# Performance work log

Hardware: AMD Instinct MI355X
Metric: run time of the kernel (lower is better)

## Reference

```python
import jax, jax.numpy as jnp
import numpy as np

CAPACITY = 2  # module init arg


def setup_inputs() -> dict:
    B, S, D, E, I = 4, 4096, 1024, 8, 4096
    key = jax.random.key(0)
    k0, k1, k2, k3, k4 = jax.random.split(key, 5)
    x = jax.random.normal(k0, (B, S, D), dtype=jnp.float32)
    # nn.init.normal_(gate_weight, std=0.006)
    gate_w = jax.random.normal(k1, (E, D), dtype=jnp.float32) * 0.006
    w_gate = jax.random.normal(k2, (E, I, D), dtype=jnp.float32) * (1.0 / np.sqrt(D))
    w_up = jax.random.normal(k3, (E, I, D), dtype=jnp.float32) * (1.0 / np.sqrt(D))
    w_down = jax.random.normal(k4, (E, D, I), dtype=jnp.float32) * (1.0 / np.sqrt(I))
    return {"x": x, "gate_w": gate_w, "w_gate": w_gate, "w_up": w_up, "w_down": w_down}


def reference(x, gate_w, w_gate, w_up, w_down):
    # Expert-choice MoE. The torch code materializes a one-hot dispatch tensor
    # (B,E,C,S) and contracts it with x / x_e; mathematically that is exactly an
    # indexed gather (dispatch) and scatter-add (combine), which we do directly.
    B, S, D = x.shape
    E = gate_w.shape[0]
    k = (S // E) * CAPACITY  # capacity per expert

    logits = jnp.einsum('bsd,ed->bse', x, gate_w)
    affinity = jax.nn.softmax(logits, axis=-1)              # softmax over experts
    affinity = jnp.transpose(affinity, (0, 2, 1))           # (B,E,S)
    gating, idx = jax.lax.top_k(affinity, k)                # each expert picks k tokens; (B,E,k)

    bidx = jnp.arange(B)[:, None, None]                     # (B,1,1) broadcast vs (B,E,k)
    x_in = x[bidx, idx]                                     # gather: (B,E,k,D)

    # per-expert gated SiLU MLP: down(silu(gate(x)) * up(x))
    h = jax.nn.silu(jnp.einsum('bekd,eid->beki', x_in, w_gate)) \
        * jnp.einsum('bekd,eid->beki', x_in, w_up)          # (B,E,k,I)
    x_e = jnp.einsum('beki,edi->bekd', h, w_down)           # (B,E,k,D)

    # combine: scatter-add gated expert outputs back to token positions
    out = jnp.zeros_like(x).at[bidx, idx].add(gating[..., None] * x_e)
    return out
```

## Files before the change

kernel.cpp:

```cpp
#include <hip/hip_runtime.h>
#include <hip/hip_bf16.h>


#define B_ 4
#define S_ 4096
#define D_ 1024
#define E_ 8
#define I_ 4096
#define KCAP 1024
#define NGROUPS 32

typedef __bf16 bf16x8 __attribute__((ext_vector_type(8)));
typedef float floatx4 __attribute__((ext_vector_type(4)));

#define GLD16(gptr, lptr)                                          \
  __builtin_amdgcn_global_load_lds(                                \
      (const __attribute__((address_space(1))) void*)(gptr),       \
      (__attribute__((address_space(3))) void*)(lptr), 16, 0, 0)

#define WAITV(N) asm volatile("s_waitcnt vmcnt(" #N ")" ::: "memory")
#define RAW_BAR() __builtin_amdgcn_s_barrier()
#define CFENCE() asm volatile("" ::: "memory")

__device__ __forceinline__ float bf2f(unsigned short h) {
  union { unsigned int u; float f; } v; v.u = ((unsigned int)h) << 16; return v.f;
}
__device__ __forceinline__ unsigned short f2bf(float f) {
  union { float f; unsigned int u; } v; v.f = f;
  unsigned int r = (v.u + 0x7fffu + ((v.u >> 16) & 1u)) >> 16;
  return (unsigned short)r;
}

__global__ __launch_bounds__(256) void probe_dtype_k(const unsigned short* __restrict__ xr,
                                                     int* __restrict__ flag) {
  __shared__ unsigned int cnt;
  if (threadIdx.x == 0) cnt = 0;
  __syncthreads();
  unsigned int local = 0;
  for (int j = 0; j < 16; ++j) {
    int k = threadIdx.x * 16 + j;
    unsigned short u = xr[2 * k];
    unsigned int expf = (u >> 7) & 0xFF;
    if (expf >= 0x90 && expf != 0xFF) local++;
    if (expf == 0xFF) local++;
  }
  atomicAdd(&cnt, local);
  __syncthreads();
  if (threadIdx.x == 0) *flag = (cnt > 256u) ? 1 : 0;
}

__global__ __launch_bounds__(256) void conv_in_k(const void* __restrict__ src,
                                                 unsigned short* __restrict__ dst,
                                                 const int* __restrict__ flag) {
  const int isf32 = *flag;
  size_t i = ((size_t)blockIdx.x * 256 + threadIdx.x) * 8;
  if (isf32) {
    const float* s = (const float*)src;
    float4 a = *(const float4*)(s + i);
    float4 b = *(const float4*)(s + i + 4);
    ushort4 o0, o1;
    o0.x = f2bf(a.x); o0.y = f2bf(a.y); o0.z = f2bf(a.z); o0.w = f2bf(a.w);
    o1.x = f2bf(b.x); o1.y = f2bf(b.y); o1.z = f2bf(b.z); o1.w = f2bf(b.w);
    *(ushort4*)(dst + i) = o0;
    *(ushort4*)(dst + i + 4) = o1;
  } else {
    const uint4* s = (const uint4*)src;
    *(uint4*)(dst + i) = s[i / 8];
  }
}

__global__ __launch_bounds__(256) void gate_softmax_k(
    const void* __restrict__ xr, const void* __restrict__ gwr,
    const int* __restrict__ flag, double* __restrict__ aff) {
  const int isf32 = *flag;
  const int wave = threadIdx.x >> 6, lane = threadIdx.x & 63;
  const int token = blockIdx.x * 4 + wave;
  double acc[E_];
#pragma unroll
  for (int e2 = 0; e2 < E_; ++e2) acc[e2] = 0.0;
  for (int j = 0; j < 16; ++j) {
    int k = lane + 64 * j;
    double xv, wv[E_];
    if (isf32) {
      xv = (double)((const float*)xr)[(size_t)token * D_ + k];
#pragma unroll
      for (int e2 = 0; e2 < E_; ++e2) wv[e2] = (double)((const float*)gwr)[e2 * D_ + k];
    } else {
      xv = (double)bf2f(((const unsigned short*)xr)[(size_t)token * D_ + k]);
#pragma unroll
      for (int e2 = 0; e2 < E_; ++e2) wv[e2] = (double)bf2f(((const unsigned short*)gwr)[e2 * D_ + k]);
    }
#pragma unroll
    for (int e2 = 0; e2 < E_; ++e2) acc[e2] += xv * wv[e2];
  }
#pragma unroll
  for (int e2 = 0; e2 < E_; ++e2) {
#pragma unroll
    for (int off = 1; off < 64; off <<= 1) acc[e2] += __shfl_xor(acc[e2], off);
  }
  if (lane < E_) {
    double mx = acc[0];
#pragma unroll
    for (int e2 = 1; e2 < E_; ++e2) mx = acc[e2] > mx ? acc[e2] : mx;
    double ssum = 0.0;
#pragma unroll
    for (int e2 = 0; e2 < E_; ++e2) ssum += exp(acc[e2] - mx);
    double p = exp(acc[lane] - mx) / ssum;
    int b = token >> 12, s = token & (S_ - 1);
    aff[((size_t)b * E_ + lane) * S_ + s] = p;
  }
}

__global__ __launch_bounds__(256) void topk_sel_k(
    const double* __restrict__ aff, int* __restrict__ sel_idx, float* __restrict__ sel_gate) {
  __shared__ unsigned long long keys[4096];
  __shared__ unsigned int hist[256];
  __shared__ unsigned int bcast[3];
  const int g = blockIdx.x, t = threadIdx.x;
  const int e = g >> 2, b = g & 3;
  const double* ap = aff + ((size_t)b * E_ + e) * S_;
  for (int j = 0; j < 16; ++j) {
    int i = t + 256 * j;
    keys[i] = __double_as_longlong(ap[i]);
  }
  __syncthreads();
  unsigned long long prefix = 0ull;
  int remaining = KCAP;
  for (int p = 7; p >= 0; --p) {
    hist[t] = 0;
    __syncthreads();
    unsigned long long mask_hi = (p == 7) ? 0ull : (~0ull << ((p + 1) * 8));
    for (int j = 0; j < 16; ++j) {
      unsigned long long key = keys[t + 256 * j];
      if ((key & mask_hi) == prefix)
        atomicAdd(&hist[(unsigned)(key >> (p * 8)) & 255u], 1u);
    }
    __syncthreads();
    if (t == 0) {
      unsigned cum = 0; int bsel = 0;
      for (int v = 255; v >= 0; --v) {
        unsigned cc = hist[v];
        if (cum + cc >= (unsigned)remaining) { bsel = v; break; }
        cum += cc;
      }
      bcast[0] = (unsigned)bsel; bcast[1] = cum;
    }
    __syncthreads();
    prefix |= ((unsigned long long)bcast[0]) << (p * 8);
    remaining -= (int)bcast[1];
    __syncthreads();
  }
  if (t == 0) bcast[2] = 0;
  __syncthreads();
  const unsigned long long T = prefix;
  for (int j = 0; j < 16; ++j) {
    int i = t + 256 * j;
    unsigned long long key = keys[i];
    if (key > T) {
      unsigned pos = atomicAdd(&bcast[2], 1u);
      sel_idx[g * KCAP + pos] = i;
      sel_gate[g * KCAP + pos] = (float)__longlong_as_double(key);
    }
  }
  __syncthreads();
  for (int j = 0; j < 16; ++j) {
    int i = t + 256 * j;
    unsigned long long key = keys[i];
    if (key == T) {
      unsigned pos = atomicAdd(&bcast[2], 1u);
      if (pos < KCAP) {
        sel_idx[g * KCAP + pos] = i;
        sel_gate[g * KCAP + pos] = (float)__longlong_as_double(key);
      }
    }
  }
}

__global__ __launch_bounds__(512, 2) void moe_gemm1(
    const unsigned short* __restrict__ x, const unsigned short* __restrict__ w_gate,
    const unsigned short* __restrict__ w_up, const int* __restrict__ sel_idx,
    unsigned short* __restrict__ hbuf, int chunk_start) {
  __shared__ __align__(16) unsigned short lds[4 * 16384];
  const int gc = blockIdx.z;
  const int g = chunk_start + gc;
  const int e = g >> 2, b = g & 3;
  const int lid = blockIdx.x;
  const int swz = (lid & 7) * 16 + (lid >> 3);
  const int m0 = (swz & 3) * 256, n0 = (swz >> 2) * 128;
  const int t = threadIdx.x;
  const int wave = t >> 6, lane = t & 63;
  const int wm = wave >> 2, wn = wave & 3;
  const int row16 = lane & 15, quad = lane >> 4;

  const int atok = sel_idx[g * KCAP + m0 + (t & 255)] & (S_ - 1);
  const unsigned short* gA = x + ((size_t)b * S_ + atok) * D_ + (t >> 8) * 8;
  const unsigned short* gG = w_gate + ((size_t)e * I_ + n0 + (t & 127)) * D_ + (t >> 7) * 8;
  const unsigned short* gU = w_up + ((size_t)e * I_ + n0 + (t & 127)) * D_ + (t >> 7) * 8;

  floatx4 accg[8][2], accu[8][2];
#pragma unroll
  for (int m = 0; m < 8; ++m)
#pragma unroll
    for (int n = 0; n < 2; ++n) {
      accg[m][n] = (floatx4){0.f, 0.f, 0.f, 0.f};
      accu[m][n] = (floatx4){0.f, 0.f, 0.f, 0.f};
    }

#define STG1(KT, SL) do {                                   \
    unsigned short* sb_ = lds + (SL) * 16384;               \
    const int k0_ = (KT) * 32;                              \
    GLD16(gA + k0_,      sb_ + wave * 512);                 \
    GLD16(gA + k0_ + 16, sb_ + 4096 + wave * 512);          \
    GLD16(gG + k0_,      sb_ + 8192 + wave * 512);          \
    GLD16(gU + k0_,      sb_ + 12288 + wave * 512);         \
  } while (0)

#define COMP1(SL) do {                                                              \
    const unsigned short* sb_ = lds + (SL) * 16384;                                 \
    bf16x8 af[8], gf[2], uf[2];                                                     \
    _Pragma("unroll")                                                               \
    for (int m = 0; m < 8; ++m)                                                     \
      af[m] = *(const bf16x8*)(sb_ + (quad * 256 + wm * 128 + m * 16 + row16) * 8); \
    _Pragma("unroll")                                                               \
    for (int n = 0; n < 2; ++n) {                                                   \
      gf[n] = *(const bf16x8*)(sb_ + 8192 + (quad * 128 + wn * 32 + n * 16 + row16) * 8);  \
      uf[n] = *(const bf16x8*)(sb_ + 12288 + (quad * 128 + wn * 32 + n * 16 + row16) * 8); \
    }                                                                               \
    __builtin_amdgcn_s_setprio(1);                                                  \
    _Pragma("unroll")                                                               \
    for (int m = 0; m < 8; ++m)                                                     \
      _Pragma("unroll")                                                             \
      for (int n = 0; n < 2; ++n) {                                                 \
        accg[m][n] = __builtin_amdgcn_mfma_f32_16x16x32_bf16(af[m], gf[n], accg[m][n], 0, 0, 0); \
        accu[m][n] = __builtin_amdgcn_mfma_f32_16x16x32_bf16(af[m], uf[n], accu[m][n], 0, 0, 0); \
      }                                                                             \
    __builtin_amdgcn_s_setprio(0);                                                  \
  } while (0)

  STG1(0, 0); CFENCE(); STG1(1, 1); CFENCE(); STG1(2, 2);
#pragma unroll 4
  for (int kt = 0; kt < 28; ++kt) {
    WAITV(8); RAW_BAR();
    STG1(kt + 3, (kt + 3) & 3);
    COMP1(kt & 3);
  }
  { WAITV(8); RAW_BAR(); STG1(31, 3); COMP1(0); }
  { WAITV(8); RAW_BAR(); COMP1(1); }
  { WAITV(4); RAW_BAR(); COMP1(2); }
  { WAITV(0); RAW_BAR(); COMP1(3); }
#undef STG1
#undef COMP1

  unsigned short* hb = hbuf + (size_t)gc * ((size_t)KCAP * I_);
#pragma unroll
  for (int m = 0; m < 8; ++m)
#pragma unroll
    for (int n = 0; n < 2; ++n)
#pragma unroll
      for (int r4 = 0; r4 < 4; ++r4) {
        int mm = m0 + wm * 128 + m * 16 + quad * 4 + r4;
        int nn = n0 + wn * 32 + n * 16 + row16;
        float gv = accg[m][n][r4], uv = accu[m][n][r4];
        float hv = gv / (1.f + __expf(-gv)) * uv;
        hb[(size_t)mm * I_ + nn] = f2bf(hv);
      }
}

__global__ __launch_bounds__(512, 2) void moe_gemm2(
    const unsigned short* __restrict__ hbuf, const unsigned short* __restrict__ w_down,
    const int* __restrict__ sel_idx, const float* __restrict__ sel_gate,
    float* __restrict__ acc_out, int chunk_start) {
  __shared__ __align__(16) unsigned short lds[4 * 16384];
  __shared__ int stok[256];
  __shared__ float sgt[256];
  const int gc = blockIdx.z;
  const int g = chunk_start + gc;
  const int e = g >> 2, b = g & 3;
  const int m0 = (blockIdx.x & 3) * 256, n0 = (blockIdx.x >> 2) * 256;
  const int t = threadIdx.x;
  const int wave = t >> 6, lane = t & 63;
  const int wm = wave >> 2, wn = wave & 3;
  const int row16 = lane & 15, quad = lane >> 4;

  if (t < 256) {
    stok[t] = sel_idx[g * KCAP + m0 + t] & (S_ - 1);
    sgt[t] = sel_gate[g * KCAP + m0 + t];
  }

  const unsigned short* gA = hbuf + (size_t)gc * ((size_t)KCAP * I_) +
                             (size_t)(m0 + (t & 255)) * I_ + (t >> 8) * 8;
  const unsigned short* gB = w_down + ((size_t)e * D_ + n0 + (t & 255)) * I_ + (t >> 8) * 8;

  floatx4 accf[8][4];
#pragma unroll
  for (int m = 0; m < 8; ++m)
#pragma unroll
    for (int n = 0; n < 4; ++n) accf[m][n] = (floatx4){0.f, 0.f, 0.f, 0.f};

#define STG2(KT, SL) do {                                   \
    unsigned short* sb_ = lds + (SL) * 16384;               \
    const int k0_ = (KT) * 32;                              \
    GLD16(gA + k0_,      sb_ + wave * 512);                 \
    GLD16(gA + k0_ + 16, sb_ + 4096 + wave * 512);          \
    GLD16(gB + k0_,      sb_ + 8192 + wave * 512);          \
    GLD16(gB + k0_ + 16, sb_ + 12288 + wave * 512);         \
  } while (0)

#define COMP2(SL) do {                                                              \
    const unsigned short* sb_ = lds + (SL) * 16384;                                 \
    bf16x8 af[8], bf[4];                                                            \
    _Pragma("unroll")                                                               \
    for (int m = 0; m < 8; ++m)                                                     \
      af[m] = *(const bf16x8*)(sb_ + (quad * 256 + wm * 128 + m * 16 + row16) * 8); \
    _Pragma("unroll")                                                               \
    for (int n = 0; n < 4; ++n)                                                     \
      bf[n] = *(const bf16x8*)(sb_ + 8192 + (quad * 256 + wn * 64 + n * 16 + row16) * 8); \
    __builtin_amdgcn_s_setprio(1);                                                  \
    _Pragma("unroll")                                                               \
    for (int m = 0; m < 8; ++m)                                                     \
      _Pragma("unroll")                                                             \
      for (int n = 0; n < 4; ++n)                                                   \
        accf[m][n] = __builtin_amdgcn_mfma_f32_16x16x32_bf16(af[m], bf[n], accf[m][n], 0, 0, 0); \
    __builtin_amdgcn_s_setprio(0);                                                  \
  } while (0)

  STG2(0, 0); CFENCE(); STG2(1, 1); CFENCE(); STG2(2, 2);
#pragma unroll 4
  for (int kt = 0; kt < 124; ++kt) {
    WAITV(8); RAW_BAR();
    STG2(kt + 3, (kt + 3) & 3);
    COMP2(kt & 3);
  }
  { WAITV(8); RAW_BAR(); STG2(127, 3); COMP2(0); }
  { WAITV(8); RAW_BAR(); COMP2(1); }
  { WAITV(4); RAW_BAR(); COMP2(2); }
  { WAITV(0); RAW_BAR(); COMP2(3); }
#undef STG2
#undef COMP2

#pragma unroll
  for (int m = 0; m < 8; ++m)
#pragma unroll
    for (int r4 = 0; r4 < 4; ++r4) {
      int mloc = wm * 128 + m * 16 + quad * 4 + r4;
      int tok = stok[mloc];
      float gt = sgt[mloc];
      float* basep = acc_out + ((size_t)b * S_ + tok) * D_ + n0 + wn * 64 + row16;
#pragma unroll
      for (int n = 0; n < 4; ++n) unsafeAtomicAdd(basep + n * 16, accf[m][n][r4] * gt);
    }
}

__global__ __launch_bounds__(256) void conv_out_k(const float* __restrict__ acc,
                                                  void* __restrict__ out,
                                                  const int* __restrict__ flag) {
  const int isf32 = *flag;
  size_t i = ((size_t)blockIdx.x * 256 + threadIdx.x) * 4;
  float4 v = *(const float4*)(acc + i);
  if (isf32) {
    *(float4*)((float*)out + i) = v;
  } else {
    ushort4 o;
    o.x = f2bf(v.x); o.y = f2bf(v.y); o.z = f2bf(v.z); o.w = f2bf(v.w);
    *(ushort4*)((unsigned short*)out + i) = o;
  }
}

extern "C" void kernel_launch(void* const* d_in, const int* in_sizes, int n_in,
                              void* d_out, int out_size, void* d_ws, size_t ws_size,
                              hipStream_t stream) {
  const void* x_raw = d_in[0];
  const void* gate_w_raw = d_in[1];
  const void* w_gate_raw = d_in[2];
  const void* w_up_raw = d_in[3];
  const void* w_down_raw = d_in[4];

  char* ws = (char*)d_ws;
  size_t off = 0;
  auto alloc = [&](size_t bytes) { char* p = ws + off; off += (bytes + 255) & ~(size_t)255; return p; };
  float* acc = (float*)alloc((size_t)B_ * S_ * D_ * 4);
  double* aff = (double*)alloc((size_t)B_ * E_ * S_ * 8);
  int* sel_idx = (int*)alloc((size_t)NGROUPS * KCAP * 4);
  float* sel_gate = (float*)alloc((size_t)NGROUPS * KCAP * 4);
  int* flag = (int*)alloc(256);
  unsigned short* xb = (unsigned short*)alloc((size_t)B_ * S_ * D_ * 2);
  unsigned short* wgb = (unsigned short*)alloc((size_t)E_ * I_ * D_ * 2);
  unsigned short* wub = (unsigned short*)alloc((size_t)E_ * I_ * D_ * 2);
  unsigned short* wdb = (unsigned short*)alloc((size_t)E_ * D_ * I_ * 2);
  const size_t fixedBytes = off;
  const size_t hPerGroup = (size_t)KCAP * I_ * 2;
  int gch = 32;
  while (gch > 1 && fixedBytes + (size_t)gch * hPerGroup > ws_size) gch >>= 1;
  unsigned short* hbuf = (unsigned short*)(ws + fixedBytes);

  hipMemsetAsync(acc, 0, (size_t)B_ * S_ * D_ * 4, stream);
  hipMemsetAsync(sel_idx, 0, (size_t)NGROUPS * KCAP * 8, stream);

  probe_dtype_k<<<dim3(1), dim3(256), 0, stream>>>((const unsigned short*)x_raw, flag);
  conv_in_k<<<dim3((int)((size_t)B_ * S_ * D_ / 2048)), dim3(256), 0, stream>>>(x_raw, xb, flag);
  conv_in_k<<<dim3((int)((size_t)E_ * I_ * D_ / 2048)), dim3(256), 0, stream>>>(w_gate_raw, wgb, flag);
  conv_in_k<<<dim3((int)((size_t)E_ * I_ * D_ / 2048)), dim3(256), 0, stream>>>(w_up_raw, wub, flag);
  conv_in_k<<<dim3((int)((size_t)E_ * D_ * I_ / 2048)), dim3(256), 0, stream>>>(w_down_raw, wdb, flag);

  gate_softmax_k<<<dim3(B_ * S_ / 4), dim3(256), 0, stream>>>(x_raw, gate_w_raw, flag, aff);
  topk_sel_k<<<dim3(NGROUPS), dim3(256), 0, stream>>>(aff, sel_idx, sel_gate);
  for (int c0 = 0; c0 < NGROUPS; c0 += gch) {
    int gcur = (NGROUPS - c0) < gch ? (NGROUPS - c0) : gch;
    moe_gemm1<<<dim3(128, 1, gcur), dim3(512), 0, stream>>>(
        xb, wgb, wub, sel_idx, hbuf, c0);
    moe_gemm2<<<dim3(16, 1, gcur), dim3(512), 0, stream>>>(
        hbuf, wdb, sel_idx, sel_gate, acc, c0);
  }
  conv_out_k<<<dim3((int)((size_t)B_ * S_ * D_ / 4 / 256)), dim3(256), 0, stream>>>(acc, d_out, flag);
}
```

Baseline: 1.951 ms.

## Split GEMM k-steps into two interleaved phases with staged loads and barriers

Both expert GEMM kernels now split each k-step into two half-tile MFMA phases. The global-to-LDS loads for a future stage are spread across the phases, and barriers plus explicit lgkmcnt waits and sched_barriers control the instruction order, in a ping-pong style schedule. Launch bounds drop from 2 to 1 block per CU, which frees registers but leaves fewer resident waves to hide latency. The tail iterations reload clamped k-slice 31/127 into spare slots, which adds redundant loads. The extra barriers per k-step add sync cost.

```diff
diff --git a/kernel.cpp b/kernel.cpp
--- a/kernel.cpp
+++ b/kernel.cpp
@@ -19,8 +19,11 @@
       (__attribute__((address_space(3))) void*)(lptr), 16, 0, 0)
 
 #define WAITV(N) asm volatile("s_waitcnt vmcnt(" #N ")" ::: "memory")
+#define LGKM0() do { asm volatile("s_waitcnt lgkmcnt(0)" ::: "memory"); \
+                     __builtin_amdgcn_sched_barrier(0); } while (0)
 #define RAW_BAR() __builtin_amdgcn_s_barrier()
 #define CFENCE() asm volatile("" ::: "memory")
+#define MFMA_BF16(A, Bb, C) __builtin_amdgcn_mfma_f32_16x16x32_bf16((A), (Bb), (C), 0, 0, 0)
 
 __device__ __forceinline__ float bf2f(unsigned short h) {
   union { unsigned int u; float f; } v; v.u = ((unsigned int)h) << 16; return v.f;
@@ -176,7 +179,7 @@
   }
 }
 
-__global__ __launch_bounds__(512, 2) void moe_gemm1(
+__global__ __launch_bounds__(512, 1) void moe_gemm1(
     const unsigned short* __restrict__ x, const unsigned short* __restrict__ w_gate,
     const unsigned short* __restrict__ w_up, const int* __restrict__ sel_idx,
     unsigned short* __restrict__ hbuf, int chunk_start) {
@@ -192,10 +195,10 @@
   const int wm = wave >> 2, wn = wave & 3;
   const int row16 = lane & 15, quad = lane >> 4;
 
-  const int atok = sel_idx[g * KCAP + m0 + (t & 255)] & (S_ - 1);
-  const unsigned short* gA = x + ((size_t)b * S_ + atok) * D_ + (t >> 8) * 8;
-  const unsigned short* gG = w_gate + ((size_t)e * I_ + n0 + (t & 127)) * D_ + (t >> 7) * 8;
-  const unsigned short* gU = w_up + ((size_t)e * I_ + n0 + (t & 127)) * D_ + (t >> 7) * 8;
+  const int tokA = sel_idx[g * KCAP + m0 + (t & 255)] & (S_ - 1);
+  const unsigned short* pA = x + ((size_t)b * S_ + tokA) * D_ + (t >> 8) * 8;
+  const unsigned short* pG = w_gate + ((size_t)e * I_ + n0 + (t & 127)) * D_ + (t >> 7) * 8;
+  const unsigned short* pU = w_up + ((size_t)e * I_ + n0 + (t & 127)) * D_ + (t >> 7) * 8;
 
   floatx4 accg[8][2], accu[8][2];
 #pragma unroll
@@ -205,51 +208,77 @@
       accg[m][n] = (floatx4){0.f, 0.f, 0.f, 0.f};
       accu[m][n] = (floatx4){0.f, 0.f, 0.f, 0.f};
     }
-
-#define STG1(KT, SL) do {                                   \
-    unsigned short* sb_ = lds + (SL) * 16384;               \
-    const int k0_ = (KT) * 32;                              \
-    GLD16(gA + k0_,      sb_ + wave * 512);                 \
-    GLD16(gA + k0_ + 16, sb_ + 4096 + wave * 512);          \
-    GLD16(gG + k0_,      sb_ + 8192 + wave * 512);          \
-    GLD16(gU + k0_,      sb_ + 12288 + wave * 512);         \
-  } while (0)
-
-#define COMP1(SL) do {                                                              \
-    const unsigned short* sb_ = lds + (SL) * 16384;                                 \
-    bf16x8 af[8], gf[2], uf[2];                                                     \
-    _Pragma("unroll")                                                               \
-    for (int m = 0; m < 8; ++m)                                                     \
-      af[m] = *(const bf16x8*)(sb_ + (quad * 256 + wm * 128 + m * 16 + row16) * 8); \
-    _Pragma("unroll")                                                               \
-    for (int n = 0; n < 2; ++n) {                                                   \
-      gf[n] = *(const bf16x8*)(sb_ + 8192 + (quad * 128 + wn * 32 + n * 16 + row16) * 8);  \
-      uf[n] = *(const bf16x8*)(sb_ + 12288 + (quad * 128 + wn * 32 + n * 16 + row16) * 8); \
-    }                                                                               \
-    __builtin_amdgcn_s_setprio(1);                                                  \
-    _Pragma("unroll")                                                               \
-    for (int m = 0; m < 8; ++m)                                                     \
-      _Pragma("unroll")                                                             \
-      for (int n = 0; n < 2; ++n) {                                                 \
-        accg[m][n] = __builtin_amdgcn_mfma_f32_16x16x32_bf16(af[m], gf[n], accg[m][n], 0, 0, 0); \
-        accu[m][n] = __builtin_amdgcn_mfma_f32_16x16x32_bf16(af[m], uf[n], accu[m][n], 0, 0, 0); \
-      }                                                                             \
-    __builtin_amdgcn_s_setprio(0);                                                  \
-  } while (0)
+  bf16x8 af[4], gf[2], uf[2];
+
+#define STG1(KT, SL) do { unsigned short* sb_ = lds + (SL) * 16384;  \
+    const int k0_ = (KT) * 32;                                       \
+    GLD16(pA + k0_,      sb_ + wave * 512);                          \
+    GLD16(pA + k0_ + 16, sb_ + 4096 + wave * 512);                   \
+    GLD16(pG + k0_,      sb_ + 8192 + wave * 512);                   \
+    GLD16(pU + k0_,      sb_ + 12288 + wave * 512); } while (0)
+
+#define PHA1(CS, SS, KS) do {                                                        \
+    const unsigned short* cb_ = lds + (CS) * 16384;                                  \
+    unsigned short* sb_ = lds + (SS) * 16384;                                        \
+    _Pragma("unroll")                                                                \
+    for (int m = 0; m < 4; ++m)                                                      \
+      af[m] = *(const bf16x8*)(cb_ + (quad * 256 + wm * 128 + m * 16 + row16) * 8);  \
+    _Pragma("unroll")                                                                \
+    for (int n = 0; n < 2; ++n) {                                                    \
+      gf[n] = *(const bf16x8*)(cb_ + 8192 + (quad * 128 + wn * 32 + n * 16 + row16) * 8);  \
+      uf[n] = *(const bf16x8*)(cb_ + 12288 + (quad * 128 + wn * 32 + n * 16 + row16) * 8); \
+    }                                                                                \
+    GLD16(pA + (KS) * 32,      sb_ + wave * 512);                                    \
+    GLD16(pA + (KS) * 32 + 16, sb_ + 4096 + wave * 512);                             \
+    RAW_BAR();                                                                       \
+    LGKM0();                                                                         \
+    __builtin_amdgcn_s_setprio(1);                                                   \
+    _Pragma("unroll")                                                                \
+    for (int m = 0; m < 4; ++m)                                                      \
+      _Pragma("unroll")                                                              \
+      for (int n = 0; n < 2; ++n) {                                                  \
+        accg[m][n] = MFMA_BF16(af[m], gf[n], accg[m][n]);                            \
+        accu[m][n] = MFMA_BF16(af[m], uf[n], accu[m][n]);                            \
+      }                                                                              \
+    __builtin_amdgcn_s_setprio(0);                                                   \
+    RAW_BAR(); } while (0)
+
+#define PHB1(CS, SS, KS) do {                                                        \
+    const unsigned short* cb_ = lds + (CS) * 16384;                                  \
+    unsigned short* sb_ = lds + (SS) * 16384;                                        \
+    _Pragma("unroll")                                                                \
+    for (int m = 0; m < 4; ++m)                                                      \
+      af[m] = *(const bf16x8*)(cb_ + (quad * 256 + wm * 128 + (m + 4) * 16 + row16) * 8); \
+    GLD16(pG + (KS) * 32, sb_ + 8192 + wave * 512);                                  \
+    GLD16(pU + (KS) * 32, sb_ + 12288 + wave * 512);                                 \
+    WAITV(8);                                                                        \
+    RAW_BAR();                                                                       \
+    LGKM0();                                                                         \
+    __builtin_amdgcn_s_setprio(1);                                                   \
+    _Pragma("unroll")                                                                \
+    for (int m = 0; m < 4; ++m)                                                      \
+      _Pragma("unroll")                                                              \
+      for (int n = 0; n < 2; ++n) {                                                  \
+        accg[m + 4][n] = MFMA_BF16(af[m], gf[n], accg[m + 4][n]);                    \
+        accu[m + 4][n] = MFMA_BF16(af[m], uf[n], accu[m + 4][n]);                    \
+      }                                                                              \
+    __builtin_amdgcn_s_setprio(0);                                                   \
+    RAW_BAR(); } while (0)
 
   STG1(0, 0); CFENCE(); STG1(1, 1); CFENCE(); STG1(2, 2);
-#pragma unroll 4
-  for (int kt = 0; kt < 28; ++kt) {
-    WAITV(8); RAW_BAR();
-    STG1(kt + 3, (kt + 3) & 3);
-    COMP1(kt & 3);
-  }
-  { WAITV(8); RAW_BAR(); STG1(31, 3); COMP1(0); }
-  { WAITV(8); RAW_BAR(); COMP1(1); }
-  { WAITV(4); RAW_BAR(); COMP1(2); }
-  { WAITV(0); RAW_BAR(); COMP1(3); }
+  WAITV(8); RAW_BAR();
+
+  for (int kt = 0; kt < 32; kt += 4) {
+    int ks;
+    ks = kt + 3 > 31 ? 31 : kt + 3;  PHA1(0, 3, ks); PHB1(0, 3, ks);
+    ks = kt + 4 > 31 ? 31 : kt + 4;  PHA1(1, 0, ks); PHB1(1, 0, ks);
+    ks = kt + 5 > 31 ? 31 : kt + 5;  PHA1(2, 1, ks); PHB1(2, 1, ks);
+    ks = kt + 6 > 31 ? 31 : kt + 6;  PHA1(3, 2, ks); PHB1(3, 2, ks);
+  }
+  WAITV(0);
 #undef STG1
-#undef COMP1
+#undef PHA1
+#undef PHB1
 
   unsigned short* hb = hbuf + (size_t)gc * ((size_t)KCAP * I_);
 #pragma unroll
@@ -266,7 +295,7 @@
       }
 }
 
-__global__ __launch_bounds__(512, 2) void moe_gemm2(
+__global__ __launch_bounds__(512, 1) void moe_gemm2(
     const unsigned short* __restrict__ hbuf, const unsigned short* __restrict__ w_down,
     const int* __restrict__ sel_idx, const float* __restrict__ sel_gate,
     float* __restrict__ acc_out, int chunk_start) {
@@ -287,56 +316,80 @@
     sgt[t] = sel_gate[g * KCAP + m0 + t];
   }
 
-  const unsigned short* gA = hbuf + (size_t)gc * ((size_t)KCAP * I_) +
+  const unsigned short* pA = hbuf + (size_t)gc * ((size_t)KCAP * I_) +
                              (size_t)(m0 + (t & 255)) * I_ + (t >> 8) * 8;
-  const unsigned short* gB = w_down + ((size_t)e * D_ + n0 + (t & 255)) * I_ + (t >> 8) * 8;
+  const unsigned short* pB = w_down + ((size_t)e * D_ + n0 + (t & 255)) * I_ + (t >> 8) * 8;
 
   floatx4 accf[8][4];
 #pragma unroll
   for (int m = 0; m < 8; ++m)
 #pragma unroll
     for (int n = 0; n < 4; ++n) accf[m][n] = (floatx4){0.f, 0.f, 0.f, 0.f};
-
-#define STG2(KT, SL) do {                                   \
-    unsigned short* sb_ = lds + (SL) * 16384;               \
-    const int k0_ = (KT) * 32;                              \
-    GLD16(gA + k0_,      sb_ + wave * 512);                 \
-    GLD16(gA + k0_ + 16, sb_ + 4096 + wave * 512);          \
-    GLD16(gB + k0_,      sb_ + 8192 + wave * 512);          \
-    GLD16(gB + k0_ + 16, sb_ + 12288 + wave * 512);         \
-  } while (0)
-
-#define COMP2(SL) do {                                                              \
-    const unsigned short* sb_ = lds + (SL) * 16384;                                 \
-    bf16x8 af[8], bf[4];                                                            \
-    _Pragma("unroll")                                                               \
-    for (int m = 0; m < 8; ++m)                                                     \
-      af[m] = *(const bf16x8*)(sb_ + (quad * 256 + wm * 128 + m * 16 + row16) * 8); \
-    _Pragma("unroll")                                                               \
-    for (int n = 0; n < 4; ++n)                                                     \
-      bf[n] = *(const bf16x8*)(sb_ + 8192 + (quad * 256 + wn * 64 + n * 16 + row16) * 8); \
-    __builtin_amdgcn_s_setprio(1);                                                  \
-    _Pragma("unroll")                                                               \
-    for (int m = 0; m < 8; ++m)                                                     \
-      _Pragma("unroll")                                                             \
-      for (int n = 0; n < 4; ++n)                                                   \
-        accf[m][n] = __builtin_amdgcn_mfma_f32_16x16x32_bf16(af[m], bf[n], accf[m][n], 0, 0, 0); \
-    __builtin_amdgcn_s_setprio(0);                                                  \
-  } while (0)
+  bf16x8 af[4], bf[4];
+
+#define STG2(KT, SL) do { unsigned short* sb_ = lds + (SL) * 16384;  \
+    const int k0_ = (KT) * 32;                                       \
+    GLD16(pA + k0_,      sb_ + wave * 512);                          \
+    GLD16(pA + k0_ + 16, sb_ + 4096 + wave * 512);                   \
+    GLD16(pB + k0_,      sb_ + 8192 + wave * 512);                   \
+    GLD16(pB + k0_ + 16, sb_ + 12288 + wave * 512); } while (0)
+
+#define PHA2(CS, SS, KS) do {                                                        \
+    const unsigned short* cb_ = lds + (CS) * 16384;                                  \
+    unsigned short* sb_ = lds + (SS) * 16384;                                        \
+    _Pragma("unroll")                                                                \
+    for (int m = 0; m < 4; ++m)                                                      \
+      af[m] = *(const bf16x8*)(cb_ + (quad * 256 + wm * 128 + m * 16 + row16) * 8);  \
+    _Pragma("unroll")                                                                \
+    for (int n = 0; n < 4; ++n)                                                      \
+      bf[n] = *(const bf16x8*)(cb_ + 8192 + (quad * 256 + wn * 64 + n * 16 + row16) * 8); \
+    GLD16(pA + (KS) * 32,      sb_ + wave * 512);                                    \
+    GLD16(pA + (KS) * 32 + 16, sb_ + 4096 + wave * 512);                             \
+    RAW_BAR();                                                                       \
+    LGKM0();                                                                         \
+    __builtin_amdgcn_s_setprio(1);                                                   \
+    _Pragma("unroll")                                                                \
+    for (int m = 0; m < 4; ++m)                                                      \
+      _Pragma("unroll")                                                              \
+      for (int n = 0; n < 4; ++n)                                                    \
+        accf[m][n] = MFMA_BF16(af[m], bf[n], accf[m][n]);                            \
+    __builtin_amdgcn_s_setprio(0);                                                   \
+    RAW_BAR(); } while (0)
+
+#define PHB2(CS, SS, KS) do {                                                        \
+    const unsigned short* cb_ = lds + (CS) * 16384;                                  \
+    unsigned short* sb_ = lds + (SS) * 16384;                                        \
+    _Pragma("unroll")                                                                \
+    for (int m = 0; m < 4; ++m)                                                      \
+      af[m] = *(const bf16x8*)(cb_ + (quad * 256 + wm * 128 + (m + 4) * 16 + row16) * 8); \
+    GLD16(pB + (KS) * 32,      sb_ + 8192 + wave * 512);                             \
+    GLD16(pB + (KS) * 32 + 16, sb_ + 12288 + wave * 512);                            \
+    WAITV(8);                                                                        \
+    RAW_BAR();                                                                       \
+    LGKM0();                                                                         \
+    __builtin_amdgcn_s_setprio(1);                                                   \
+    _Pragma("unroll")                                                                \
+    for (int m = 0; m < 4; ++m)                                                      \
+      _Pragma("unroll")                                                              \
+      for (int n = 0; n < 4; ++n)                                                    \
+        accf[m + 4][n] = MFMA_BF16(af[m], bf[n], accf[m + 4][n]);                    \
+    __builtin_amdgcn_s_setprio(0);                                                   \
+    RAW_BAR(); } while (0)
 
   STG2(0, 0); CFENCE(); STG2(1, 1); CFENCE(); STG2(2, 2);
-#pragma unroll 4
-  for (int kt = 0; kt < 124; ++kt) {
-    WAITV(8); RAW_BAR();
-    STG2(kt + 3, (kt + 3) & 3);
-    COMP2(kt & 3);
-  }
-  { WAITV(8); RAW_BAR(); STG2(127, 3); COMP2(0); }
-  { WAITV(8); RAW_BAR(); COMP2(1); }
-  { WAITV(4); RAW_BAR(); COMP2(2); }
-  { WAITV(0); RAW_BAR(); COMP2(3); }
+  WAITV(8); RAW_BAR();
+
+  for (int kt = 0; kt < 128; kt += 4) {
+    int ks;
+    ks = kt + 3 > 127 ? 127 : kt + 3;  PHA2(0, 3, ks); PHB2(0, 3, ks);
+    ks = kt + 4 > 127 ? 127 : kt + 4;  PHA2(1, 0, ks); PHB2(1, 0, ks);
+    ks = kt + 5 > 127 ? 127 : kt + 5;  PHA2(2, 1, ks); PHB2(2, 1, ks);
+    ks = kt + 6 > 127 ? 127 : kt + 6;  PHA2(3, 2, ks); PHB2(3, 2, ks);
+  }
+  WAITV(0);
 #undef STG2
-#undef COMP2
+#undef PHA2
+#undef PHB2
 
 #pragma unroll
   for (int m = 0; m < 8; ++m)
```

After: 1.915 ms. Within noise of the previous version (-1.9%).
